# Kernel tuning notes

Hardware: AMD Instinct MI355X
Metric: run time of the kernel (lower is better)

Reference implementation:

```python
import jax, jax.numpy as jnp
import numpy as np
from jax import lax

FEAT_STRIDE = 16
RATIOS = np.array([0.5, 1.0, 2.0], np.float32)
SCALES = np.array([8.0, 16.0, 32.0], np.float32)
A = RATIOS.size * SCALES.size            # 9 anchors per location
N_PRE = 3000                             # pre-NMS top-k (TEST-style config)
N_POST = 300                             # post-NMS rois per image
NMS_THRESH = 0.7
MIN_SIZE = 16.0
B, C, HF, WF = 4, 512, 50, 50


def setup_inputs() -> dict:
    key = jax.random.key(0)
    ks = jax.random.split(key, 4)
    mid = 512
    return {
        "inputs": jax.random.normal(ks[0], (B, C, HF, WF), jnp.float32),
        "conv_w": jax.random.normal(ks[1], (mid, C, 3, 3), jnp.float32) * 0.01,
        "conv_b": jnp.zeros((mid,), jnp.float32),
        "bf_w": jax.random.normal(ks[2], (A * 2, mid, 1, 1), jnp.float32) * 0.01,
        "bf_b": jnp.zeros((A * 2,), jnp.float32),
        "loc_w": jax.random.normal(ks[3], (A * 4, mid, 1, 1), jnp.float32) * 0.01,
        "loc_b": jnp.zeros((A * 4,), jnp.float32),
        "img_h": 800,
        "img_w": 800,
    }


def _conv(x, w, b, pad):
    y = lax.conv_general_dilated(x, w, (1, 1), [(pad, pad), (pad, pad)],
                                 dimension_numbers=("NCHW", "OIHW", "NCHW"))
    return y + b[None, :, None, None]


def _anchors(hf, wf):
    ratios = jnp.asarray(RATIOS)
    scales = jnp.asarray(SCALES)
    hs = (FEAT_STRIDE * scales[None, :] * jnp.sqrt(ratios[:, None])).reshape(-1)
    ws = (FEAT_STRIDE * scales[None, :] * jnp.sqrt(1.0 / ratios[:, None])).reshape(-1)
    c = FEAT_STRIDE / 2.0
    base = jnp.stack([c - hs / 2, c - ws / 2, c + hs / 2, c + ws / 2], 1)  # [A,4] yxyx
    sy = jnp.arange(hf, dtype=jnp.float32) * FEAT_STRIDE
    sx = jnp.arange(wf, dtype=jnp.float32) * FEAT_STRIDE
    yy, xx = jnp.meshgrid(sy, sx, indexing="ij")
    shifts = jnp.stack([yy, xx, yy, xx], -1).reshape(-1, 1, 4)
    return (shifts + base[None]).reshape(-1, 4)  # [hf*wf*A, 4]


def _decode(anchors, loc):
    # anchors [N,4] yxyx, loc [B,N,4] (dy,dx,dh,dw)
    ah = anchors[:, 2] - anchors[:, 0]
    aw = anchors[:, 3] - anchors[:, 1]
    acy = anchors[:, 0] + 0.5 * ah
    acx = anchors[:, 1] + 0.5 * aw
    cy = loc[..., 0] * ah + acy
    cx = loc[..., 1] * aw + acx
    h = jnp.exp(loc[..., 2]) * ah
    w = jnp.exp(loc[..., 3]) * aw
    return jnp.stack([cy - 0.5 * h, cx - 0.5 * w, cy + 0.5 * h, cx + 0.5 * w], -1)


def _nms(boxes, scores):
    # boxes [N,4], scores [N] -> fixed-size [N_POST,4] rois (zero-padded)
    hs = boxes[:, 2] - boxes[:, 0]
    ws = boxes[:, 3] - boxes[:, 1]
    valid = (hs >= MIN_SIZE) & (ws >= MIN_SIZE)
    s = jnp.where(valid, scores, -jnp.inf)
    order = jnp.argsort(-s)[:N_PRE]
    b = boxes[order]
    v = valid[order]
    sb = lax.stop_gradient(b)
    area = (sb[:, 2] - sb[:, 0]) * (sb[:, 3] - sb[:, 1])
    tl = jnp.maximum(sb[:, None, :2], sb[None, :, :2])
    br = jnp.minimum(sb[:, None, 2:], sb[None, :, 2:])
    wh = jnp.clip(br - tl, 0.0)
    inter = wh[..., 0] * wh[..., 1]
    iou = inter / (area[:, None] + area[None, :] - inter + 1e-9)

    def body(i, keep):
        sup = jnp.any((iou[i] > NMS_THRESH) & keep)
        return keep.at[i].set(v[i] & ~sup)

    keep = lax.fori_loop(0, N_PRE, body, jnp.zeros((N_PRE,), bool))
    pos = jnp.where(keep, jnp.cumsum(keep) - 1, N_POST)  # invalid -> dropped
    return jnp.zeros((N_POST, 4), boxes.dtype).at[pos].set(b, mode="drop")


def reference(inputs, conv_w, conv_b, bf_w, bf_b, loc_w, loc_b, img_h, img_w):
    b_, _, hf, wf = inputs.shape
    feat = jax.nn.relu(_conv(inputs, conv_w, conv_b, 1))
    loc = _conv(feat, loc_w, loc_b, 0).transpose(0, 2, 3, 1).reshape(b_, -1, 4)
    logits = _conv(feat, bf_w, bf_b, 0).transpose(0, 2, 3, 1).reshape(b_, hf, wf, A, 2)
    probs = jax.nn.softmax(logits, axis=4)
    fg = probs[..., 1].reshape(b_, -1)             # foreground scores [B, hf*wf*A]
    bf_pred = probs.reshape(b_, -1, 2)
    anchors = _anchors(hf, wf)
    boxes = _decode(anchors, loc)
    boxes = jnp.stack([
        jnp.clip(boxes[..., 0], 0.0, img_h), jnp.clip(boxes[..., 1], 0.0, img_w),
        jnp.clip(boxes[..., 2], 0.0, img_h), jnp.clip(boxes[..., 3], 0.0, img_w)], -1)
    rois = jax.vmap(_nms)(boxes, fg).reshape(-1, 4)         # [B*N_POST, 4]
    rois_idx = jnp.repeat(jnp.arange(b_, dtype=jnp.int32), N_POST)
    return rois, rois_idx, anchors, loc, bf_pred
```

## Files before the change

### kernel.cpp

```cpp
#include <hip/hip_runtime.h>
#include <hip/hip_bf16.h>
#include <math.h>

#define BIMG   4
#define CIN    512
#define MID    512
#define HF     50
#define WF     50
#define PIX    2500
#define MTOT   10000
#define ANC    9
#define NLOC   22500
#define NPRE   3000
#define NPOST  300
#define WORDS  47
#define ROWPAD 3008
#define WSTRIDE 48
#define CAP    8192

#define ROIS_OFF 0
#define IDX_OFF  4800
#define ANC_OFF  6000
#define LOC_OFF  96000
#define BF_OFF   456000

#define WS_WT     0UL
#define WS_W1T    9437184UL
#define WS_FEAT   9568256UL
#define WS_SCORE  30048256UL
#define WS_BOXD   30768256UL
#define WS_SBD    33648256UL
#define WS_M      34032256UL
#define WS_CAND   38652544UL
#define WS_CNT    38783616UL
#define WS_THR    38783632UL

__global__ __launch_bounds__(256) void prep_kernel(
    const float* __restrict__ conv_w, const float* __restrict__ loc_w,
    const float* __restrict__ bf_w, float* __restrict__ Wt, float* __restrict__ W1t) {
  int o = blockIdx.x * 256 + threadIdx.x;
  if (o < 4608 * 512) {
    int co  = o & 511;
    int k   = o >> 9;
    int c   = k & 511;
    int tap = k >> 9;
    Wt[o] = conv_w[(co * 512 + c) * 9 + tap];
  } else {
    int o2 = o - 4608 * 512;
    if (o2 < 512 * 64) {
      int co = o2 & 63;
      int c  = o2 >> 6;
      float v = 0.0f;
      if (co < 36)      v = loc_w[co * 512 + c];
      else if (co < 54) v = bf_w[(co - 36) * 512 + c];
      W1t[o2] = v;
    }
  }
}

__device__ __forceinline__ void stage_load(
    int kb, int sg, bool in0, bool in1,
    int y0, int x0, int y1, int x1,
    const float* __restrict__ ib0, const float* __restrict__ ib1, float av[8]) {
  int tap = kb >> 5;
  int c0  = (kb & 31) << 4;
  int t3  = tap / 3;
  int dy  = t3 - 1;
  int dx  = tap - t3 * 3 - 1;
  int iy0 = y0 + dy, ix0 = x0 + dx;
  int iy1 = y1 + dy, ix1 = x1 + dx;
  bool ok0 = in0 && ((unsigned)iy0 < (unsigned)HF) && ((unsigned)ix0 < (unsigned)WF);
  bool ok1 = in1 && ((unsigned)iy1 < (unsigned)HF) && ((unsigned)ix1 < (unsigned)WF);
  int base = (c0 + sg * 4) * PIX;
  int o0 = iy0 * WF + ix0;
  int o1 = iy1 * WF + ix1;
#pragma unroll
  for (int j = 0; j < 4; ++j) {
    av[2 * j]     = ok0 ? ib0[base + j * PIX + o0] : 0.0f;
    av[2 * j + 1] = ok1 ? ib1[base + j * PIX + o1] : 0.0f;
  }
}

__global__ __launch_bounds__(256, 3) void conv3x3_kernel(
    const float* __restrict__ in, const float* __restrict__ Wt,
    const float* __restrict__ bias, float* __restrict__ feat) {
  __shared__ float As[2][16][128];
  const int tid = threadIdx.x;
  const int q0 = blockIdx.x * 128;
  const int lane = tid & 63;
  const int wv = tid >> 6;
  const int col0 = __builtin_amdgcn_readfirstlane(blockIdx.y * 64 + wv * 16);

  const int sg = tid >> 6;
  const int sp = tid & 63;
  int qs0 = q0 + 2 * sp, qs1 = qs0 + 1;
  bool in0 = qs0 < MTOT, in1 = qs1 < MTOT;
  int t0 = in0 ? qs0 : 0, t1 = in1 ? qs1 : 0;
  int b0i = t0 / PIX, r0 = t0 - b0i * PIX, y0 = r0 / WF, x0 = r0 - y0 * WF;
  int b1i = t1 / PIX, r1 = t1 - b1i * PIX, y1 = r1 / WF, x1 = r1 - y1 * WF;
  const float* ib0 = in + (size_t)b0i * (CIN * PIX);
  const float* ib1 = in + (size_t)b1i * (CIN * PIX);

  double acc[2][16];
  float accf[2][16];
#pragma unroll
  for (int p = 0; p < 2; ++p)
#pragma unroll
    for (int c = 0; c < 16; ++c) { acc[p][c] = 0.0; accf[p][c] = 0.0f; }

  {
    float av[8];
    stage_load(0, sg, in0, in1, y0, x0, y1, x1, ib0, ib1, av);
#pragma unroll
    for (int j = 0; j < 4; ++j)
      *(float2*)&As[0][sg * 4 + j][2 * sp] = make_float2(av[2 * j], av[2 * j + 1]);
  }
  __syncthreads();

  for (int kb = 0; kb < 288; ++kb) {
    int cur = kb & 1;
    float av[8];
    bool has_next = (kb + 1 < 288);
    if (has_next)
      stage_load(kb + 1, sg, in0, in1, y0, x0, y1, x1, ib0, ib1, av);

    const float* __restrict__ Bw = Wt + (size_t)(kb * 16) * 512 + col0;
#pragma unroll
    for (int kg = 0; kg < 4; ++kg) {
#pragma unroll
      for (int kq = 0; kq < 4; ++kq) {
        int kk = kg * 4 + kq;
        const float* __restrict__ br = Bw + (size_t)kk * 512;
        float2 a = *(const float2*)&As[cur][kk][2 * lane];
#pragma unroll
        for (int c = 0; c < 16; ++c) {
          float bv = br[c];
          accf[0][c] = fmaf(a.x, bv, accf[0][c]);
          accf[1][c] = fmaf(a.y, bv, accf[1][c]);
        }
      }
    }
    if (kb & 1) {
#pragma unroll
      for (int p = 0; p < 2; ++p)
#pragma unroll
        for (int c = 0; c < 16; ++c) {
          acc[p][c] += (double)accf[p][c];
          accf[p][c] = 0.0f;
        }
    }
    if (has_next) {
      int nxt = cur ^ 1;
#pragma unroll
      for (int j = 0; j < 4; ++j)
        *(float2*)&As[nxt][sg * 4 + j][2 * sp] = make_float2(av[2 * j], av[2 * j + 1]);
    }
    __syncthreads();
  }

  double bd[16];
#pragma unroll
  for (int c = 0; c < 16; ++c) bd[c] = (double)bias[col0 + c];
#pragma unroll
  for (int p = 0; p < 2; ++p) {
    int q = q0 + 2 * lane + p;
    if (q < MTOT) {
      float o[16];
#pragma unroll
      for (int c = 0; c < 16; ++c)
        o[c] = (float)fmax(acc[p][c] + bd[c], 0.0);
      float* fp = &feat[(size_t)q * 512 + col0];
#pragma unroll
      for (int g = 0; g < 4; ++g)
        *(float4*)&fp[g * 4] = make_float4(o[g*4], o[g*4+1], o[g*4+2], o[g*4+3]);
    }
  }
}

__global__ __launch_bounds__(256) void conv1x1_kernel(
    const float* __restrict__ feat, const float* __restrict__ W1t,
    const float* __restrict__ locb, const float* __restrict__ bfb,
    double* __restrict__ rawd) {
  __shared__ float As[16][128];
  const int tid = threadIdx.x;
  const int q0 = blockIdx.x * 128;
  const int lane = tid & 63;
  const int wv = tid >> 6;
  const int col0 = __builtin_amdgcn_readfirstlane(wv * 16);

  const int pixL = tid >> 1;
  const int ch   = (tid & 1) * 8;
  const int qL   = q0 + pixL;
  const bool okL = qL < MTOT;

  double acc[2][16];
  float accf[2][16];
#pragma unroll
  for (int p = 0; p < 2; ++p)
#pragma unroll
    for (int c = 0; c < 16; ++c) { acc[p][c] = 0.0; accf[p][c] = 0.0f; }

  for (int kb = 0; kb < 32; ++kb) {
    int c0 = kb * 16;
    float4 f0 = make_float4(0, 0, 0, 0), f1 = make_float4(0, 0, 0, 0);
    if (okL) {
      const float* fp = &feat[(size_t)qL * 512 + c0 + ch];
      f0 = *(const float4*)fp;
      f1 = *(const float4*)(fp + 4);
    }
    __syncthreads();
    As[ch + 0][pixL] = f0.x; As[ch + 1][pixL] = f0.y;
    As[ch + 2][pixL] = f0.z; As[ch + 3][pixL] = f0.w;
    As[ch + 4][pixL] = f1.x; As[ch + 5][pixL] = f1.y;
    As[ch + 6][pixL] = f1.z; As[ch + 7][pixL] = f1.w;
    __syncthreads();

    const float* __restrict__ Bw = W1t + (size_t)c0 * 64 + col0;
#pragma unroll
    for (int kk = 0; kk < 16; ++kk) {
      const float* __restrict__ br = Bw + (size_t)kk * 64;
      float2 a = *(const float2*)&As[kk][2 * lane];
#pragma unroll
      for (int c = 0; c < 16; ++c) {
        float bv = br[c];
        accf[0][c] = fmaf(a.x, bv, accf[0][c]);
        accf[1][c] = fmaf(a.y, bv, accf[1][c]);
      }
    }
    if (kb & 1) {
#pragma unroll
      for (int p = 0; p < 2; ++p)
#pragma unroll
        for (int c = 0; c < 16; ++c) {
          acc[p][c] += (double)accf[p][c];
          accf[p][c] = 0.0f;
        }
    }
  }

  double bs[16];
#pragma unroll
  for (int c = 0; c < 16; ++c) {
    int co = col0 + c;
    bs[c] = (co < 36) ? (double)locb[co] : ((co < 54) ? (double)bfb[co - 36] : 0.0);
  }
#pragma unroll
  for (int p = 0; p < 2; ++p) {
    int q = q0 + 2 * lane + p;
    if (q < MTOT) {
      double* rp = &rawd[(size_t)q * 64 + col0];
#pragma unroll
      for (int c = 0; c < 16; ++c) rp[c] = acc[p][c] + bs[c];
    }
  }
}

__global__ __launch_bounds__(256) void epilogue_kernel(
    const double* __restrict__ rawd, float* __restrict__ d_out,
    double* __restrict__ boxd, unsigned long long* __restrict__ ukey,
    const int* __restrict__ imh, const int* __restrict__ imw) {
  int idx = blockIdx.x * 256 + threadIdx.x;
  if (idx >= BIMG * NLOC) return;
  int b = idx / NLOC;
  int i = idx - b * NLOC;
  int p = i / ANC;
  int a = i - p * ANC;
  int y = p / WF;
  int x = p - y * WF;
  int q = b * PIX + p;

  double l0d = rawd[(size_t)q * 64 + a * 4 + 0];
  double l1d = rawd[(size_t)q * 64 + a * 4 + 1];
  double l2d = rawd[(size_t)q * 64 + a * 4 + 2];
  double l3d = rawd[(size_t)q * 64 + a * 4 + 3];
  float4 lo = make_float4((float)l0d, (float)l1d, (float)l2d, (float)l3d);
  *(float4*)&d_out[LOC_OFF + (size_t)idx * 4] = lo;

  double g0 = rawd[(size_t)q * 64 + 36 + a * 2];
  double g1 = rawd[(size_t)q * 64 + 37 + a * 2];
  double m  = fmax(g0, g1);
  double e0 = exp(g0 - m), e1 = exp(g1 - m);
  double s  = e0 + e1;
  double p0 = e0 / s, p1 = e1 / s;
  *(float2*)&d_out[BF_OFF + (size_t)idx * 2] = make_float2((float)p0, (float)p1);

  int ridx = a / 3, sidx = a - ridx * 3;
  double ratio = (ridx == 0) ? 0.5 : ((ridx == 1) ? 1.0 : 2.0);
  double scale = (sidx == 0) ? 8.0 : ((sidx == 1) ? 16.0 : 32.0);
  double hs = 16.0 * scale * sqrt(ratio);
  double ws = 16.0 * scale * sqrt(1.0 / ratio);
  double sy = (double)(y * 16), sx = (double)(x * 16);
  double a0 = sy + (8.0 - hs * 0.5);
  double a1 = sx + (8.0 - ws * 0.5);
  double a2 = sy + (8.0 + hs * 0.5);
  double a3 = sx + (8.0 + ws * 0.5);
  if (b == 0) {
    *(float4*)&d_out[ANC_OFF + (size_t)i * 4] =
        make_float4((float)a0, (float)a1, (float)a2, (float)a3);
  }

  double ah = a2 - a0, aw = a3 - a1;
  double acy = a0 + 0.5 * ah, acx = a1 + 0.5 * aw;
  double cy = l0d * ah + acy;
  double cx = l1d * aw + acx;
  double hh = exp(l2d) * ah;
  double ww = exp(l3d) * aw;
  double ihf = (double)imh[0], iwf = (double)imw[0];
  double b0 = fmin(fmax(cy - 0.5 * hh, 0.0), ihf);
  double b1 = fmin(fmax(cx - 0.5 * ww, 0.0), iwf);
  double b2 = fmin(fmax(cy + 0.5 * hh, 0.0), ihf);
  double b3 = fmin(fmax(cx + 0.5 * ww, 0.0), iwf);
  double* bp = &boxd[(size_t)idx * 4];
  bp[0] = b0; bp[1] = b1; bp[2] = b2; bp[3] = b3;

  bool valid = (b2 - b0 >= 16.0) && (b3 - b1 >= 16.0);
  double d = valid ? (g1 - g0) : -INFINITY;
  long long bits = __double_as_longlong(d);
  unsigned long long u = (bits < 0)
      ? ~(unsigned long long)bits
      : ((unsigned long long)bits | 0x8000000000000000ull);
  ukey[idx] = ~u;
}

__global__ __launch_bounds__(1024) void thresh_kernel(
    const unsigned long long* __restrict__ ukey,
    unsigned* __restrict__ thr, unsigned* __restrict__ ccnt) {
  __shared__ unsigned hist[16384];
  __shared__ unsigned csum[1024];
  int b = blockIdx.x;
  int tid = threadIdx.x;
  for (int i = tid; i < 16384; i += 1024) hist[i] = 0;
  __syncthreads();
  for (int j = tid; j < NLOC; j += 1024)
    atomicAdd(&hist[(unsigned)(ukey[(size_t)b * NLOC + j] >> 50)], 1u);
  __syncthreads();
  unsigned s = 0;
#pragma unroll
  for (int k = 0; k < 16; ++k) s += hist[tid * 16 + k];
  csum[tid] = s;
  __syncthreads();
  if (tid == 0) {
    unsigned cum = 0;
    int T = 16383;
    for (int c = 0; c < 1024; ++c) {
      if (cum + csum[c] >= NPRE) {
        unsigned cc = cum;
        for (int k = 0; k < 16; ++k) {
          cc += hist[c * 16 + k];
          if (cc >= NPRE) { T = c * 16 + k; break; }
        }
        break;
      }
      cum += csum[c];
    }
    thr[b] = (unsigned)T;
    ccnt[b] = 0;
  }
}

__global__ __launch_bounds__(256) void compact_kernel(
    const unsigned long long* __restrict__ ukey, const unsigned* __restrict__ thr,
    unsigned* __restrict__ ccnt, unsigned* __restrict__ cand) {
  int b = blockIdx.y;
  int i = blockIdx.x * 256 + threadIdx.x;
  if (i >= NLOC) return;
  unsigned T = thr[b];
  if ((unsigned)(ukey[(size_t)b * NLOC + i] >> 50) <= T) {
    unsigned slot = atomicAdd(&ccnt[b], 1u);
    if (slot < CAP) cand[(size_t)b * CAP + slot] = (unsigned)i;
  }
}

__global__ __launch_bounds__(256) void rank_kernel(
    const unsigned long long* __restrict__ ukey, const unsigned* __restrict__ ccnt,
    const unsigned* __restrict__ cand, const double* __restrict__ boxd,
    double* __restrict__ sbd) {
  __shared__ unsigned long long kt[256];
  __shared__ unsigned it[256];
  int b = blockIdx.y;
  int C = (int)min(ccnt[b], (unsigned)CAP);
  int s = blockIdx.x * 256 + threadIdx.x;
  bool act = s < C;
  unsigned myi = act ? cand[(size_t)b * CAP + s] : 0xFFFFFFFFu;
  unsigned long long ki = act ? ukey[(size_t)b * NLOC + myi] : ~0ull;
  int cnt = 0;
  int ntile = (C + 255) >> 8;
  for (int t = 0; t < ntile; ++t) {
    int j = t * 256 + threadIdx.x;
    unsigned ji = (j < C) ? cand[(size_t)b * CAP + j] : 0xFFFFFFFFu;
    kt[threadIdx.x] = (j < C) ? ukey[(size_t)b * NLOC + ji] : ~0ull;
    it[threadIdx.x] = ji;
    __syncthreads();
#pragma unroll 8
    for (int jj = 0; jj < 256; ++jj) {
      unsigned long long kj = kt[jj];
      unsigned jidx = it[jj];
      cnt += ((kj < ki) || (kj == ki && jidx < myi)) ? 1 : 0;
    }
    __syncthreads();
  }
  if (act && cnt < NPRE) {
    const double* bx = &boxd[((size_t)b * NLOC + myi) * 4];
    double* dp = &sbd[((size_t)b * NPRE + cnt) * 4];
    dp[0] = bx[0]; dp[1] = bx[1]; dp[2] = bx[2]; dp[3] = bx[3];
  }
}

__global__ __launch_bounds__(64) void nmsmask_kernel(
    const double* __restrict__ sbd, unsigned long long* __restrict__ M) {
  __shared__ double cb[64][4];
  int b = blockIdx.z;
  int jw = blockIdx.y;
  int i  = blockIdx.x * 64 + threadIdx.x;
  int j  = jw * 64 + threadIdx.x;
  double j0 = 0, j1 = 0, j2 = 0, j3 = 0;
  if (j < NPRE) {
    const double* bp = &sbd[((size_t)b * NPRE + j) * 4];
    j0 = bp[0]; j1 = bp[1]; j2 = bp[2]; j3 = bp[3];
  }
  cb[threadIdx.x][0] = j0; cb[threadIdx.x][1] = j1;
  cb[threadIdx.x][2] = j2; cb[threadIdx.x][3] = j3;
  __syncthreads();
  if (i >= NPRE) return;
  const double* bp = &sbd[((size_t)b * NPRE + i) * 4];
  double i0 = bp[0], i1 = bp[1], i2 = bp[2], i3 = bp[3];
  double ai = (i2 - i0) * (i3 - i1);
  unsigned long long mask = 0ull;
#pragma unroll 4
  for (int t = 0; t < 64; ++t) {
    double aj = (cb[t][2] - cb[t][0]) * (cb[t][3] - cb[t][1]);
    double h = fmax(fmin(i2, cb[t][2]) - fmax(i0, cb[t][0]), 0.0);
    double w = fmax(fmin(i3, cb[t][3]) - fmax(i1, cb[t][1]), 0.0);
    double inter = h * w;
    double iou = inter / (ai + aj - inter + 1e-9);
    mask |= ((iou > 0.7) ? 1ull : 0ull) << t;
  }
  M[((size_t)b * ROWPAD + i) * WSTRIDE + jw] = mask;
}

__global__ __launch_bounds__(64) void nms_scan_kernel(
    const double* __restrict__ sbd, const unsigned long long* __restrict__ M,
    float* __restrict__ d_out) {
  int b = blockIdx.x;
  int lane = threadIdx.x;
  for (int k = lane; k < NPOST; k += 64) {
    *(float4*)&d_out[ROIS_OFF + (size_t)(b * NPOST + k) * 4] = make_float4(0, 0, 0, 0);
    d_out[IDX_OFF + b * NPOST + k] = (float)b;
  }
  __syncthreads();

  unsigned long long R = ~0ull;
  if (lane < WORDS) R = 0ull;
  for (int w = 0; w < WORDS; ++w) {
    int j = w * 64 + lane;
    bool inval = true;
    if (j < NPRE) {
      const double* bp = &sbd[((size_t)b * NPRE + j) * 4];
      double h = bp[2] - bp[0], wd = bp[3] - bp[1];
      inval = !(h >= 16.0 && wd >= 16.0);
    }
    unsigned long long bal = __ballot(inval ? 1 : 0);
    if (lane == w) R |= bal;
  }

  int kept = 0;
  while (kept < NPOST) {
    unsigned long long hz = __ballot(((~R) != 0ull) ? 1 : 0);
    if (hz == 0ull) break;
    int w0 = __ffsll(hz) - 1;
    unsigned long long word = __shfl(R, w0);
    int bit = __ffsll(~word) - 1;
    int i = w0 * 64 + bit;
    if (lane < 4)
      d_out[ROIS_OFF + (size_t)(b * NPOST + kept) * 4 + lane] =
          (float)sbd[((size_t)b * NPRE + i) * 4 + lane];
    kept++;
    if (kept >= NPOST) break;
    unsigned long long row = (lane < WORDS)
        ? M[((size_t)b * ROWPAD + i) * WSTRIDE + lane] : 0ull;
    R |= row;
    if (lane == w0) R |= (1ull << bit);
  }
}

extern "C" void kernel_launch(void* const* d_in, const int* in_sizes, int n_in,
                              void* d_out, int out_size, void* d_ws, size_t ws_size,
                              hipStream_t stream) {
  const float* in     = (const float*)d_in[0];
  const float* conv_w = (const float*)d_in[1];
  const float* conv_b = (const float*)d_in[2];
  const float* bf_w   = (const float*)d_in[3];
  const float* bf_b   = (const float*)d_in[4];
  const float* loc_w  = (const float*)d_in[5];
  const float* loc_b  = (const float*)d_in[6];
  const int*   imh    = (const int*)d_in[7];
  const int*   imw    = (const int*)d_in[8];
  float* out = (float*)d_out;

  char* ws = (char*)d_ws;
  float*  Wt    = (float*)(ws + WS_WT);
  double* rawd  = (double*)(ws + WS_WT);
  float*  W1t   = (float*)(ws + WS_W1T);
  float*  feat  = (float*)(ws + WS_FEAT);
  unsigned long long* ukey = (unsigned long long*)(ws + WS_SCORE);
  double* boxd  = (double*)(ws + WS_BOXD);
  double* sbd   = (double*)(ws + WS_SBD);
  unsigned long long* M = (unsigned long long*)(ws + WS_M);
  unsigned* cand = (unsigned*)(ws + WS_CAND);
  unsigned* ccnt = (unsigned*)(ws + WS_CNT);
  unsigned* thr  = (unsigned*)(ws + WS_THR);

  hipLaunchKernelGGL(prep_kernel, dim3((4608 * 512 + 512 * 64 + 255) / 256), dim3(256),
                     0, stream, conv_w, loc_w, bf_w, Wt, W1t);
  hipLaunchKernelGGL(conv3x3_kernel, dim3(79, 8), dim3(256), 0, stream,
                     in, Wt, conv_b, feat);
  hipLaunchKernelGGL(conv1x1_kernel, dim3(79), dim3(256), 0, stream,
                     feat, W1t, loc_b, bf_b, rawd);
  hipLaunchKernelGGL(epilogue_kernel, dim3((BIMG * NLOC + 255) / 256), dim3(256), 0, stream,
                     rawd, out, boxd, ukey, imh, imw);
  hipLaunchKernelGGL(thresh_kernel, dim3(4), dim3(1024), 0, stream, ukey, thr, ccnt);
  hipLaunchKernelGGL(compact_kernel, dim3(88, 4), dim3(256), 0, stream,
                     ukey, thr, ccnt, cand);
  hipLaunchKernelGGL(rank_kernel, dim3(CAP / 256, 4), dim3(256), 0, stream,
                     ukey, ccnt, cand, boxd, sbd);
  hipLaunchKernelGGL(nmsmask_kernel, dim3(47, 47, 4), dim3(64), 0, stream, sbd, M);
  hipLaunchKernelGGL(nms_scan_kernel, dim3(4), dim3(64), 0, stream, sbd, M, out);
}
```

Before: 1.555 ms.

## Halve conv3x3 tile to one pixel per thread and fuse compaction into threshold

The 3x3 conv kernel now computes one output pixel per thread instead of two. Its M-tile drops from 128 to 64, the grid doubles to 157x8, and launch bounds rise to 4 blocks per SM, aiming at higher occupancy and better balance across the GPU's compute units. The cost is that each weight value loaded from global/L1 now feeds half as many FMAs. Separately, the candidate compaction is folded into the threshold kernel using a shared-memory counter, removing one launch and the global threshold buffer. Only 4 blocks then scan the keys serially, which may be slower than the wide compact grid.

```diff
diff --git a/kernel.cpp b/kernel.cpp
--- a/kernel.cpp
+++ b/kernel.cpp
@@ -33,7 +33,6 @@
 #define WS_M      34032256UL
 #define WS_CAND   38652544UL
 #define WS_CNT    38783616UL
-#define WS_THR    38783632UL
 
 __global__ __launch_bounds__(256) void prep_kernel(
     const float* __restrict__ conv_w, const float* __restrict__ loc_w,
@@ -59,70 +58,57 @@
 }
 
 __device__ __forceinline__ void stage_load(
-    int kb, int sg, bool in0, bool in1,
-    int y0, int x0, int y1, int x1,
-    const float* __restrict__ ib0, const float* __restrict__ ib1, float av[8]) {
+    int kb, int sg, bool inq, int y, int x,
+    const float* __restrict__ ib, float av[4]) {
   int tap = kb >> 5;
   int c0  = (kb & 31) << 4;
   int t3  = tap / 3;
   int dy  = t3 - 1;
   int dx  = tap - t3 * 3 - 1;
-  int iy0 = y0 + dy, ix0 = x0 + dx;
-  int iy1 = y1 + dy, ix1 = x1 + dx;
-  bool ok0 = in0 && ((unsigned)iy0 < (unsigned)HF) && ((unsigned)ix0 < (unsigned)WF);
-  bool ok1 = in1 && ((unsigned)iy1 < (unsigned)HF) && ((unsigned)ix1 < (unsigned)WF);
-  int base = (c0 + sg * 4) * PIX;
-  int o0 = iy0 * WF + ix0;
-  int o1 = iy1 * WF + ix1;
-#pragma unroll
-  for (int j = 0; j < 4; ++j) {
-    av[2 * j]     = ok0 ? ib0[base + j * PIX + o0] : 0.0f;
-    av[2 * j + 1] = ok1 ? ib1[base + j * PIX + o1] : 0.0f;
-  }
-}
-
-__global__ __launch_bounds__(256, 3) void conv3x3_kernel(
+  int iy = y + dy, ix = x + dx;
+  bool ok = inq && ((unsigned)iy < (unsigned)HF) && ((unsigned)ix < (unsigned)WF);
+  int base = (c0 + sg * 4) * PIX + iy * WF + ix;
+#pragma unroll
+  for (int j = 0; j < 4; ++j)
+    av[j] = ok ? ib[base + j * PIX] : 0.0f;
+}
+
+__global__ __launch_bounds__(256, 4) void conv3x3_kernel(
     const float* __restrict__ in, const float* __restrict__ Wt,
     const float* __restrict__ bias, float* __restrict__ feat) {
-  __shared__ float As[2][16][128];
+  __shared__ float As[2][16][64];
   const int tid = threadIdx.x;
-  const int q0 = blockIdx.x * 128;
+  const int q0 = blockIdx.x * 64;
   const int lane = tid & 63;
   const int wv = tid >> 6;
   const int col0 = __builtin_amdgcn_readfirstlane(blockIdx.y * 64 + wv * 16);
 
   const int sg = tid >> 6;
   const int sp = tid & 63;
-  int qs0 = q0 + 2 * sp, qs1 = qs0 + 1;
-  bool in0 = qs0 < MTOT, in1 = qs1 < MTOT;
-  int t0 = in0 ? qs0 : 0, t1 = in1 ? qs1 : 0;
-  int b0i = t0 / PIX, r0 = t0 - b0i * PIX, y0 = r0 / WF, x0 = r0 - y0 * WF;
-  int b1i = t1 / PIX, r1 = t1 - b1i * PIX, y1 = r1 / WF, x1 = r1 - y1 * WF;
-  const float* ib0 = in + (size_t)b0i * (CIN * PIX);
-  const float* ib1 = in + (size_t)b1i * (CIN * PIX);
-
-  double acc[2][16];
-  float accf[2][16];
-#pragma unroll
-  for (int p = 0; p < 2; ++p)
-#pragma unroll
-    for (int c = 0; c < 16; ++c) { acc[p][c] = 0.0; accf[p][c] = 0.0f; }
+  int qs = q0 + sp;
+  bool inq = qs < MTOT;
+  int tq = inq ? qs : 0;
+  int bi = tq / PIX, r = tq - bi * PIX, y = r / WF, x = r - y * WF;
+  const float* ib = in + (size_t)bi * (CIN * PIX);
+
+  double acc[16];
+  float accf[16];
+#pragma unroll
+  for (int c = 0; c < 16; ++c) { acc[c] = 0.0; accf[c] = 0.0f; }
 
   {
-    float av[8];
-    stage_load(0, sg, in0, in1, y0, x0, y1, x1, ib0, ib1, av);
-#pragma unroll
-    for (int j = 0; j < 4; ++j)
-      *(float2*)&As[0][sg * 4 + j][2 * sp] = make_float2(av[2 * j], av[2 * j + 1]);
+    float av[4];
+    stage_load(0, sg, inq, y, x, ib, av);
+#pragma unroll
+    for (int j = 0; j < 4; ++j) As[0][sg * 4 + j][sp] = av[j];
   }
   __syncthreads();
 
   for (int kb = 0; kb < 288; ++kb) {
     int cur = kb & 1;
-    float av[8];
+    float av[4];
     bool has_next = (kb + 1 < 288);
-    if (has_next)
-      stage_load(kb + 1, sg, in0, in1, y0, x0, y1, x1, ib0, ib1, av);
+    if (has_next) stage_load(kb + 1, sg, inq, y, x, ib, av);
 
     const float* __restrict__ Bw = Wt + (size_t)(kb * 16) * 512 + col0;
 #pragma unroll
@@ -131,29 +117,23 @@
       for (int kq = 0; kq < 4; ++kq) {
         int kk = kg * 4 + kq;
         const float* __restrict__ br = Bw + (size_t)kk * 512;
-        float2 a = *(const float2*)&As[cur][kk][2 * lane];
-#pragma unroll
-        for (int c = 0; c < 16; ++c) {
-          float bv = br[c];
-          accf[0][c] = fmaf(a.x, bv, accf[0][c]);
-          accf[1][c] = fmaf(a.y, bv, accf[1][c]);
-        }
+        float a = As[cur][kk][lane];
+#pragma unroll
+        for (int c = 0; c < 16; ++c)
+          accf[c] = fmaf(a, br[c], accf[c]);
       }
     }
     if (kb & 1) {
 #pragma unroll
-      for (int p = 0; p < 2; ++p)
-#pragma unroll
-        for (int c = 0; c < 16; ++c) {
-          acc[p][c] += (double)accf[p][c];
-          accf[p][c] = 0.0f;
-        }
+      for (int c = 0; c < 16; ++c) {
+        acc[c] += (double)accf[c];
+        accf[c] = 0.0f;
+      }
     }
     if (has_next) {
       int nxt = cur ^ 1;
 #pragma unroll
-      for (int j = 0; j < 4; ++j)
-        *(float2*)&As[nxt][sg * 4 + j][2 * sp] = make_float2(av[2 * j], av[2 * j + 1]);
+      for (int j = 0; j < 4; ++j) As[nxt][sg * 4 + j][sp] = av[j];
     }
     __syncthreads();
   }
@@ -161,19 +141,16 @@
   double bd[16];
 #pragma unroll
   for (int c = 0; c < 16; ++c) bd[c] = (double)bias[col0 + c];
-#pragma unroll
-  for (int p = 0; p < 2; ++p) {
-    int q = q0 + 2 * lane + p;
-    if (q < MTOT) {
-      float o[16];
-#pragma unroll
-      for (int c = 0; c < 16; ++c)
-        o[c] = (float)fmax(acc[p][c] + bd[c], 0.0);
-      float* fp = &feat[(size_t)q * 512 + col0];
-#pragma unroll
-      for (int g = 0; g < 4; ++g)
-        *(float4*)&fp[g * 4] = make_float4(o[g*4], o[g*4+1], o[g*4+2], o[g*4+3]);
-    }
+  int q = q0 + lane;
+  if (q < MTOT) {
+    float o[16];
+#pragma unroll
+    for (int c = 0; c < 16; ++c)
+      o[c] = (float)fmax(acc[c] + bd[c], 0.0);
+    float* fp = &feat[(size_t)q * 512 + col0];
+#pragma unroll
+    for (int g = 0; g < 4; ++g)
+      *(float4*)&fp[g * 4] = make_float4(o[g*4], o[g*4+1], o[g*4+2], o[g*4+3]);
   }
 }
 
@@ -324,12 +301,14 @@
 
 __global__ __launch_bounds__(1024) void thresh_kernel(
     const unsigned long long* __restrict__ ukey,
-    unsigned* __restrict__ thr, unsigned* __restrict__ ccnt) {
+    unsigned* __restrict__ ccnt, unsigned* __restrict__ cand) {
   __shared__ unsigned hist[16384];
   __shared__ unsigned csum[1024];
+  __shared__ unsigned sT, scnt;
   int b = blockIdx.x;
   int tid = threadIdx.x;
   for (int i = tid; i < 16384; i += 1024) hist[i] = 0;
+  if (tid == 0) scnt = 0;
   __syncthreads();
   for (int j = tid; j < NLOC; j += 1024)
     atomicAdd(&hist[(unsigned)(ukey[(size_t)b * NLOC + j] >> 50)], 1u);
@@ -353,22 +332,18 @@
       }
       cum += csum[c];
     }
-    thr[b] = (unsigned)T;
-    ccnt[b] = 0;
-  }
-}
-
-__global__ __launch_bounds__(256) void compact_kernel(
-    const unsigned long long* __restrict__ ukey, const unsigned* __restrict__ thr,
-    unsigned* __restrict__ ccnt, unsigned* __restrict__ cand) {
-  int b = blockIdx.y;
-  int i = blockIdx.x * 256 + threadIdx.x;
-  if (i >= NLOC) return;
-  unsigned T = thr[b];
-  if ((unsigned)(ukey[(size_t)b * NLOC + i] >> 50) <= T) {
-    unsigned slot = atomicAdd(&ccnt[b], 1u);
-    if (slot < CAP) cand[(size_t)b * CAP + slot] = (unsigned)i;
-  }
+    sT = (unsigned)T;
+  }
+  __syncthreads();
+  unsigned T = sT;
+  for (int j = tid; j < NLOC; j += 1024) {
+    if ((unsigned)(ukey[(size_t)b * NLOC + j] >> 50) <= T) {
+      unsigned slot = atomicAdd(&scnt, 1u);
+      if (slot < CAP) cand[(size_t)b * CAP + slot] = (unsigned)j;
+    }
+  }
+  __syncthreads();
+  if (tid == 0) ccnt[b] = scnt;
 }
 
 __global__ __launch_bounds__(256) void rank_kernel(
@@ -508,19 +483,16 @@
   unsigned long long* M = (unsigned long long*)(ws + WS_M);
   unsigned* cand = (unsigned*)(ws + WS_CAND);
   unsigned* ccnt = (unsigned*)(ws + WS_CNT);
-  unsigned* thr  = (unsigned*)(ws + WS_THR);
 
   hipLaunchKernelGGL(prep_kernel, dim3((4608 * 512 + 512 * 64 + 255) / 256), dim3(256),
                      0, stream, conv_w, loc_w, bf_w, Wt, W1t);
-  hipLaunchKernelGGL(conv3x3_kernel, dim3(79, 8), dim3(256), 0, stream,
+  hipLaunchKernelGGL(conv3x3_kernel, dim3(157, 8), dim3(256), 0, stream,
                      in, Wt, conv_b, feat);
   hipLaunchKernelGGL(conv1x1_kernel, dim3(79), dim3(256), 0, stream,
                      feat, W1t, loc_b, bf_b, rawd);
   hipLaunchKernelGGL(epilogue_kernel, dim3((BIMG * NLOC + 255) / 256), dim3(256), 0, stream,
                      rawd, out, boxd, ukey, imh, imw);
-  hipLaunchKernelGGL(thresh_kernel, dim3(4), dim3(1024), 0, stream, ukey, thr, ccnt);
-  hipLaunchKernelGGL(compact_kernel, dim3(88, 4), dim3(256), 0, stream,
-                     ukey, thr, ccnt, cand);
+  hipLaunchKernelGGL(thresh_kernel, dim3(4), dim3(1024), 0, stream, ukey, ccnt, cand);
   hipLaunchKernelGGL(rank_kernel, dim3(CAP / 256, 4), dim3(256), 0, stream,
                      ukey, ccnt, cand, boxd, sbd);
   hipLaunchKernelGGL(nmsmask_kernel, dim3(47, 47, 4), dim3(64), 0, stream, sbd, M);
```

Result: slower. 1.847 ms (+18.8%).

## Split conv3x3 reduction across grid z and fuse compaction into threshold kernel

Applied to the files above, without the earlier changes.

The 3x3 conv's 288-step K loop is split across two z-slices of the grid, each writing a partial sum. A new combine kernel adds the partials in double precision, applies bias and ReLU, and writes the feature map. This doubles the block count (79x8 was only 632 blocks) to fill more compute units, at the cost of an extra pass over the 20 MB partial buffer. The compact kernel is folded into the threshold kernel using a shared-memory counter, removing one launch. The split is only used when the workspace is large enough.

```diff
diff --git a/kernel.cpp b/kernel.cpp
--- a/kernel.cpp
+++ b/kernel.cpp
@@ -33,7 +33,8 @@
 #define WS_M      34032256UL
 #define WS_CAND   38652544UL
 #define WS_CNT    38783616UL
-#define WS_THR    38783632UL
+#define WS_PART1  38786048UL
+#define WS_NEED_SPLIT (WS_PART1 + 20480000UL)
 
 __global__ __launch_bounds__(256) void prep_kernel(
     const float* __restrict__ conv_w, const float* __restrict__ loc_w,
@@ -83,13 +84,16 @@
 
 __global__ __launch_bounds__(256, 3) void conv3x3_kernel(
     const float* __restrict__ in, const float* __restrict__ Wt,
-    const float* __restrict__ bias, float* __restrict__ feat) {
+    float* __restrict__ part0, float* __restrict__ part1) {
   __shared__ float As[2][16][128];
   const int tid = threadIdx.x;
   const int q0 = blockIdx.x * 128;
   const int lane = tid & 63;
   const int wv = tid >> 6;
   const int col0 = __builtin_amdgcn_readfirstlane(blockIdx.y * 64 + wv * 16);
+  const int half = 288 / gridDim.z;
+  const int kb0 = blockIdx.z * half;
+  float* __restrict__ dst = (blockIdx.z == 0) ? part0 : part1;
 
   const int sg = tid >> 6;
   const int sp = tid & 63;
@@ -110,17 +114,18 @@
 
   {
     float av[8];
-    stage_load(0, sg, in0, in1, y0, x0, y1, x1, ib0, ib1, av);
+    stage_load(kb0, sg, in0, in1, y0, x0, y1, x1, ib0, ib1, av);
 #pragma unroll
     for (int j = 0; j < 4; ++j)
       *(float2*)&As[0][sg * 4 + j][2 * sp] = make_float2(av[2 * j], av[2 * j + 1]);
   }
   __syncthreads();
 
-  for (int kb = 0; kb < 288; ++kb) {
-    int cur = kb & 1;
+  for (int kbl = 0; kbl < half; ++kbl) {
+    int kb = kb0 + kbl;
+    int cur = kbl & 1;
     float av[8];
-    bool has_next = (kb + 1 < 288);
+    bool has_next = (kbl + 1 < half);
     if (has_next)
       stage_load(kb + 1, sg, in0, in1, y0, x0, y1, x1, ib0, ib1, av);
 
@@ -140,7 +145,7 @@
         }
       }
     }
-    if (kb & 1) {
+    if (kbl & 1) {
 #pragma unroll
       for (int p = 0; p < 2; ++p)
 #pragma unroll
@@ -158,23 +163,40 @@
     __syncthreads();
   }
 
-  double bd[16];
-#pragma unroll
-  for (int c = 0; c < 16; ++c) bd[c] = (double)bias[col0 + c];
 #pragma unroll
   for (int p = 0; p < 2; ++p) {
     int q = q0 + 2 * lane + p;
     if (q < MTOT) {
       float o[16];
 #pragma unroll
-      for (int c = 0; c < 16; ++c)
-        o[c] = (float)fmax(acc[p][c] + bd[c], 0.0);
-      float* fp = &feat[(size_t)q * 512 + col0];
+      for (int c = 0; c < 16; ++c) o[c] = (float)acc[p][c];
+      float* fp = &dst[(size_t)q * 512 + col0];
 #pragma unroll
       for (int g = 0; g < 4; ++g)
         *(float4*)&fp[g * 4] = make_float4(o[g*4], o[g*4+1], o[g*4+2], o[g*4+3]);
     }
   }
+}
+
+__global__ __launch_bounds__(256) void combine_kernel(
+    const float* __restrict__ p0, const float* __restrict__ p1,
+    const float* __restrict__ bias, float* __restrict__ feat, int nz) {
+  int i = blockIdx.x * 256 + threadIdx.x;
+  if (i >= MTOT * 128) return;
+  int c0 = (i & 127) << 2;
+  float4 a = ((const float4*)p0)[i];
+  float4 bs = *(const float4*)&bias[c0];
+  double sx = (double)a.x, sy = (double)a.y, sz = (double)a.z, sw = (double)a.w;
+  if (nz > 1) {
+    float4 b = ((const float4*)p1)[i];
+    sx += (double)b.x; sy += (double)b.y; sz += (double)b.z; sw += (double)b.w;
+  }
+  float4 o;
+  o.x = (float)fmax(sx + (double)bs.x, 0.0);
+  o.y = (float)fmax(sy + (double)bs.y, 0.0);
+  o.z = (float)fmax(sz + (double)bs.z, 0.0);
+  o.w = (float)fmax(sw + (double)bs.w, 0.0);
+  ((float4*)feat)[i] = o;
 }
 
 __global__ __launch_bounds__(256) void conv1x1_kernel(
@@ -324,12 +346,14 @@
 
 __global__ __launch_bounds__(1024) void thresh_kernel(
     const unsigned long long* __restrict__ ukey,
-    unsigned* __restrict__ thr, unsigned* __restrict__ ccnt) {
+    unsigned* __restrict__ ccnt, unsigned* __restrict__ cand) {
   __shared__ unsigned hist[16384];
   __shared__ unsigned csum[1024];
+  __shared__ unsigned sT, scnt;
   int b = blockIdx.x;
   int tid = threadIdx.x;
   for (int i = tid; i < 16384; i += 1024) hist[i] = 0;
+  if (tid == 0) scnt = 0;
   __syncthreads();
   for (int j = tid; j < NLOC; j += 1024)
     atomicAdd(&hist[(unsigned)(ukey[(size_t)b * NLOC + j] >> 50)], 1u);
@@ -353,22 +377,18 @@
       }
       cum += csum[c];
     }
-    thr[b] = (unsigned)T;
-    ccnt[b] = 0;
-  }
-}
-
-__global__ __launch_bounds__(256) void compact_kernel(
-    const unsigned long long* __restrict__ ukey, const unsigned* __restrict__ thr,
-    unsigned* __restrict__ ccnt, unsigned* __restrict__ cand) {
-  int b = blockIdx.y;
-  int i = blockIdx.x * 256 + threadIdx.x;
-  if (i >= NLOC) return;
-  unsigned T = thr[b];
-  if ((unsigned)(ukey[(size_t)b * NLOC + i] >> 50) <= T) {
-    unsigned slot = atomicAdd(&ccnt[b], 1u);
-    if (slot < CAP) cand[(size_t)b * CAP + slot] = (unsigned)i;
-  }
+    sT = (unsigned)T;
+  }
+  __syncthreads();
+  unsigned T = sT;
+  for (int j = tid; j < NLOC; j += 1024) {
+    if ((unsigned)(ukey[(size_t)b * NLOC + j] >> 50) <= T) {
+      unsigned slot = atomicAdd(&scnt, 1u);
+      if (slot < CAP) cand[(size_t)b * CAP + slot] = (unsigned)j;
+    }
+  }
+  __syncthreads();
+  if (tid == 0) ccnt[b] = scnt;
 }
 
 __global__ __launch_bounds__(256) void rank_kernel(
@@ -508,19 +528,21 @@
   unsigned long long* M = (unsigned long long*)(ws + WS_M);
   unsigned* cand = (unsigned*)(ws + WS_CAND);
   unsigned* ccnt = (unsigned*)(ws + WS_CNT);
-  unsigned* thr  = (unsigned*)(ws + WS_THR);
+  float*  part1 = (float*)(ws + WS_PART1);
+
+  const int nz = (ws_size >= WS_NEED_SPLIT) ? 2 : 1;
 
   hipLaunchKernelGGL(prep_kernel, dim3((4608 * 512 + 512 * 64 + 255) / 256), dim3(256),
                      0, stream, conv_w, loc_w, bf_w, Wt, W1t);
-  hipLaunchKernelGGL(conv3x3_kernel, dim3(79, 8), dim3(256), 0, stream,
-                     in, Wt, conv_b, feat);
+  hipLaunchKernelGGL(conv3x3_kernel, dim3(79, 8, nz), dim3(256), 0, stream,
+                     in, Wt, feat, part1);
+  hipLaunchKernelGGL(combine_kernel, dim3((MTOT * 128 + 255) / 256), dim3(256), 0, stream,
+                     feat, part1, conv_b, feat, nz);
   hipLaunchKernelGGL(conv1x1_kernel, dim3(79), dim3(256), 0, stream,
                      feat, W1t, loc_b, bf_b, rawd);
   hipLaunchKernelGGL(epilogue_kernel, dim3((BIMG * NLOC + 255) / 256), dim3(256), 0, stream,
                      rawd, out, boxd, ukey, imh, imw);
-  hipLaunchKernelGGL(thresh_kernel, dim3(4), dim3(1024), 0, stream, ukey, thr, ccnt);
-  hipLaunchKernelGGL(compact_kernel, dim3(88, 4), dim3(256), 0, stream,
-                     ukey, thr, ccnt, cand);
+  hipLaunchKernelGGL(thresh_kernel, dim3(4), dim3(1024), 0, stream, ukey, ccnt, cand);
   hipLaunchKernelGGL(rank_kernel, dim3(CAP / 256, 4), dim3(256), 0, stream,
                      ukey, ccnt, cand, boxd, sbd);
   hipLaunchKernelGGL(nmsmask_kernel, dim3(47, 47, 4), dim3(64), 0, stream, sbd, M);
```

After: 1.402 ms. 9.8% less time.
